# Performance work log

Hardware: AMD Instinct MI355X
Metric: run time of the kernel (lower is better)

## Reference

```python
import jax, jax.numpy as jnp
import numpy as np

VOCAB = 50257
DIM = 256


def _positional_table(seq_len, dim, dtype=jnp.float32):
    # pe[i, d] = sin(i / 10000**(d/dim))       if d even
    #          = cos(i / 10000**((d-1)/dim))   if d odd
    pos = jnp.arange(seq_len, dtype=dtype)[:, None]          # [S, 1]
    d = jnp.arange(dim)                                       # [D]
    exponent = (d - (d % 2)).astype(dtype) / dim              # d or d-1, over dim
    inv_freq = jnp.power(jnp.asarray(10000.0, dtype), -exponent)  # [D]
    angle = pos * inv_freq                                    # [S, D]
    return jnp.where(d % 2 == 0, jnp.sin(angle), jnp.cos(angle))


def setup_inputs() -> dict:
    key = jax.random.key(0)
    k1, k2 = jax.random.split(key)
    x = jax.random.randint(k1, (32, 4096), 0, VOCAB)          # token ids [B, S]
    W = jax.random.normal(k2, (VOCAB, DIM), dtype=jnp.float32)  # embedding table
    return {"x": x, "W": W}


def reference(x, W):
    # word embedding gather + sinusoidal positional encoding, broadcast over batch
    seq_len = x.shape[1]
    pe = _positional_table(seq_len, W.shape[1], W.dtype)      # [S, D]
    return W[x] + pe[None, :, :]                              # [B, S, D]
```

## Files before the change

### kernel.cpp

```cpp
#include <hip/hip_runtime.h>


#define SEQ   4096
#define DIM   256
#define BATCH 32
#define D4    (DIM / 4)

__global__ __launch_bounds__(256)
void pwe_kernel(const int* __restrict__ x,
                const float4* __restrict__ W4,
                float4* __restrict__ out4) {
    int tid = blockIdx.x * blockDim.x + threadIdx.x;
    if (tid >= SEQ * D4) return;
    int s  = tid >> 6;
    int d4 = tid & 63;
    int d0 = d4 * 4;

    float f0 = powf(10000.0f, -(float)d0       / (float)DIM);
    float f2 = powf(10000.0f, -(float)(d0 + 2) / (float)DIM);
    float p  = (float)s;
    float s0, c0, s2, c2;
    sincosf(p * f0, &s0, &c0);
    sincosf(p * f2, &s2, &c2);
    float4 pe;
    pe.x = s0; pe.y = c0; pe.z = s2; pe.w = c2;

    #pragma unroll 8
    for (int b = 0; b < BATCH; ++b) {
        int token = x[b * SEQ + s];
        float4 w = W4[(size_t)token * D4 + d4];
        float4 o;
        o.x = w.x + pe.x;
        o.y = w.y + pe.y;
        o.z = w.z + pe.z;
        o.w = w.w + pe.w;
        out4[((size_t)b * SEQ + s) * D4 + d4] = o;
    }
}

extern "C" void kernel_launch(void* const* d_in, const int* in_sizes, int n_in,
                              void* d_out, int out_size, void* d_ws, size_t ws_size,
                              hipStream_t stream) {
    const int*   x = (const int*)d_in[0];
    const float* W = (const float*)d_in[1];
    float*     out = (float*)d_out;

    const int total = SEQ * D4;
    const int block = 256;
    const int grid  = (total + block - 1) / block;
    pwe_kernel<<<grid, block, 0, stream>>>(x, (const float4*)W, (float4*)out);
}
```

Before: 205.3 us.

## Split batch across threads, batch token loads, use nontemporal output stores

```diff
diff --git a/kernel.cpp b/kernel.cpp
--- a/kernel.cpp
+++ b/kernel.cpp
@@ -5,16 +5,22 @@
 #define DIM   256
 #define BATCH 32
 #define D4    (DIM / 4)
+#define BPT   4
+#define NGRP  (BATCH / BPT)
+#define SD    (SEQ * D4)
+
+typedef float f32x4 __attribute__((ext_vector_type(4)));
 
 __global__ __launch_bounds__(256)
 void pwe_kernel(const int* __restrict__ x,
-                const float4* __restrict__ W4,
-                float4* __restrict__ out4) {
+                const f32x4* __restrict__ W4,
+                f32x4* __restrict__ out4) {
     int tid = blockIdx.x * blockDim.x + threadIdx.x;
-    if (tid >= SEQ * D4) return;
-    int s  = tid >> 6;
-    int d4 = tid & 63;
-    int d0 = d4 * 4;
+    int sd  = tid & (SD - 1);
+    int bg  = tid >> 18;
+    int s   = sd >> 6;
+    int d4  = sd & 63;
+    int d0  = d4 * 4;
 
     float f0 = powf(10000.0f, -(float)d0       / (float)DIM);
     float f2 = powf(10000.0f, -(float)(d0 + 2) / (float)DIM);
@@ -22,19 +28,22 @@
     float s0, c0, s2, c2;
     sincosf(p * f0, &s0, &c0);
     sincosf(p * f2, &s2, &c2);
-    float4 pe;
+    f32x4 pe;
     pe.x = s0; pe.y = c0; pe.z = s2; pe.w = c2;
 
-    #pragma unroll 8
-    for (int b = 0; b < BATCH; ++b) {
-        int token = x[b * SEQ + s];
-        float4 w = W4[(size_t)token * D4 + d4];
-        float4 o;
-        o.x = w.x + pe.x;
-        o.y = w.y + pe.y;
-        o.z = w.z + pe.z;
-        o.w = w.w + pe.w;
-        out4[((size_t)b * SEQ + s) * D4 + d4] = o;
+    const int b0 = bg * BPT;
+
+    int tok[BPT];
+    #pragma unroll
+    for (int i = 0; i < BPT; ++i)
+        tok[i] = x[(b0 + i) * SEQ + s];
+
+    #pragma unroll
+    for (int i = 0; i < BPT; ++i) {
+        f32x4 w = W4[(size_t)tok[i] * D4 + d4];
+        f32x4 o = w + pe;
+        __builtin_nontemporal_store(
+            o, &out4[((size_t)(b0 + i) * SEQ + s) * D4 + d4]);
     }
 }
 
@@ -45,8 +54,8 @@
     const float* W = (const float*)d_in[1];
     float*     out = (float*)d_out;
 
-    const int total = SEQ * D4;
+    const int total = SD * NGRP;
     const int block = 256;
-    const int grid  = (total + block - 1) / block;
-    pwe_kernel<<<grid, block, 0, stream>>>(x, (const float4*)W, (float4*)out);
+    const int grid  = total / block;
+    pwe_kernel<<<grid, block, 0, stream>>>(x, (const f32x4*)W, (f32x4*)out);
 }
```

After: 184.2 us. 1.11x faster.
